# Performance work log

Hardware: AMD Instinct MI355X
Metric: run time of the kernel (lower is better)

Reference implementation:

```python
import jax, jax.numpy as jnp
import numpy as np

NEG_SLOPE_ATT = 0.2   # GATv2Conv attention leaky_relu slope
NEG_SLOPE_ACT = 0.01  # F.leaky_relu default between layers


def gatv2_layer(x, src, dst, edge_attr, Wl, Wr, We, att, concat):
    """PyG GATv2Conv (bias=False, residual=False, share_weights=False,
    add_self_loops=True with fill_value='mean' for edge_attr, eval mode)."""
    N = x.shape[0]
    H, C = att.shape
    E = src.shape[0]
    # self-loop edge attrs: mean of incoming edge attrs per node (fill_value='mean')
    deg = jax.ops.segment_sum(jnp.ones((E,), x.dtype), dst, num_segments=N)
    loop_attr = jax.ops.segment_sum(edge_attr, dst, num_segments=N) / jnp.maximum(deg, 1.0)[:, None]
    loop = jnp.arange(N)
    s = jnp.concatenate([src, loop])
    d = jnp.concatenate([dst, loop])
    ea = jnp.concatenate([edge_attr, loop_attr], axis=0)
    xl = (x @ Wl).reshape(N, H, C)  # lin_l -> source features (messages)
    xr = (x @ Wr).reshape(N, H, C)  # lin_r -> target features
    # edge-wise attention input: x_l[j] + x_r[i] + lin_edge(e_ij)  -> [E+N, H, C]
    e = xl[s] + xr[d] + (ea @ We).reshape(-1, H, C)
    e = jax.nn.leaky_relu(e, NEG_SLOPE_ATT)
    logits = jnp.einsum('ehc,hc->eh', e, att)  # [E+N, H]
    # numerically stable segment softmax over incoming edges per destination
    lmax = jax.ops.segment_max(logits, d, num_segments=N)  # every node has a self loop -> finite
    ex = jnp.exp(logits - lmax[d])
    denom = jax.ops.segment_sum(ex, d, num_segments=N)
    alpha = ex / (denom[d] + 1e-16)
    out = jax.ops.segment_sum(alpha[:, :, None] * xl[s], d, num_segments=N)  # [N, H, C]
    return out.reshape(N, H * C) if concat else out.mean(axis=1)


def setup_inputs() -> dict:
    key = jax.random.key(0)
    ks = jax.random.split(key, 12)
    N, E, F, H, C, EDIM, NCLS = 50000, 800000, 128, 4, 32, 16, 1
    HC = H * C  # 128
    sc = 0.1
    return {
        'x': jax.random.normal(ks[0], (N, F), jnp.float32),
        'edge_index': jax.random.randint(ks[1], (2, E), 0, N),
        'edge_attr': jax.random.normal(ks[2], (E, EDIM), jnp.float32),
        'Wl1': jax.random.normal(ks[3], (F, HC), jnp.float32) * sc,
        'Wr1': jax.random.normal(ks[4], (F, HC), jnp.float32) * sc,
        'We1': jax.random.normal(ks[5], (EDIM, HC), jnp.float32) * sc,
        'att1': jax.random.normal(ks[6], (H, C), jnp.float32) * sc,
        'Wl2': jax.random.normal(ks[7], (HC, H * NCLS), jnp.float32) * sc,
        'Wr2': jax.random.normal(ks[8], (HC, H * NCLS), jnp.float32) * sc,
        'We2': jax.random.normal(ks[9], (EDIM, H * NCLS), jnp.float32) * sc,
        'att2': jax.random.normal(ks[10], (H, NCLS), jnp.float32) * sc,
    }


def reference(x, edge_index, edge_attr, Wl1, Wr1, We1, att1, Wl2, Wr2, We2, att2):
    src, dst = edge_index[0], edge_index[1]
    h = gatv2_layer(x, src, dst, edge_attr, Wl1, Wr1, We1, att1, concat=True)
    h = jax.nn.leaky_relu(h, NEG_SLOPE_ACT)
    out = gatv2_layer(h, src, dst, edge_attr, Wl2, Wr2, We2, att2, concat=False)
    return out.reshape(-1)
```

## Files before the change

kernel.cpp:

```cpp
#include <hip/hip_runtime.h>
#include <math.h>


typedef __attribute__((ext_vector_type(8))) short bf16x8;
typedef __attribute__((ext_vector_type(4))) float f32x4;
typedef __attribute__((ext_vector_type(2))) float f32x2;
typedef _Float16 f16;
typedef __attribute__((ext_vector_type(2))) _Float16 f16x2;
typedef __attribute__((ext_vector_type(8))) _Float16 f16x8;

static __device__ __forceinline__ ushort f2bf(float f) {
    unsigned u = __float_as_uint(f);
    unsigned r = (u + 0x7fffu + ((u >> 16) & 1u)) >> 16;
    return (ushort)r;
}

static __device__ __forceinline__ float row_sum16(float x) {
    x += __int_as_float(__builtin_amdgcn_update_dpp(0, __float_as_int(x), 0x121, 0xf, 0xf, true));
    x += __int_as_float(__builtin_amdgcn_update_dpp(0, __float_as_int(x), 0x122, 0xf, 0xf, true));
    x += __int_as_float(__builtin_amdgcn_update_dpp(0, __float_as_int(x), 0x124, 0xf, 0xf, true));
    x += __int_as_float(__builtin_amdgcn_update_dpp(0, __float_as_int(x), 0x128, 0xf, 0xf, true));
    return x;
}

static __device__ __forceinline__ float red64(float x) {
    x = row_sum16(x);
    x += __shfl_xor(x, 16);
    x += __shfl_xor(x, 32);
    return x;
}

__global__ void k_count_deg(const int* __restrict__ dst, int* __restrict__ deg, int E) {
    int i = blockIdx.x * blockDim.x + threadIdx.x;
    if (i < E) atomicAdd(&deg[dst[i]], 1);
}

__global__ __launch_bounds__(1024) void k_scan1(const int* __restrict__ deg,
                                                int* __restrict__ rowptr,
                                                int* __restrict__ part, int N) {
    __shared__ int wsum[16];
    int t = threadIdx.x, l = t & 63, w = t >> 6;
    int i = blockIdx.x * 1024 + t;
    int v = (i < N) ? deg[i] : 0;
    int sc = v;
    #pragma unroll
    for (int off = 1; off < 64; off <<= 1) {
        int y = __shfl_up(sc, off);
        if (l >= off) sc += y;
    }
    if (l == 63) wsum[w] = sc;
    __syncthreads();
    if (w == 0) {
        int pv = (l < 16) ? wsum[l] : 0;
        int psc = pv;
        #pragma unroll
        for (int off = 1; off < 16; off <<= 1) {
            int y = __shfl_up(psc, off);
            if (l >= off) psc += y;
        }
        if (l < 16) wsum[l] = psc - pv;
    }
    __syncthreads();
    if (i < N) rowptr[i] = wsum[w] + sc - v;
    if (t == 1023) part[blockIdx.x] = wsum[15] + sc;
}

__global__ void k_scan2(int* __restrict__ part, int nb) {
    int l = threadIdx.x & 63;
    int run = 0;
    for (int base = 0; base < nb; base += 64) {
        int i = base + l;
        int v = (i < nb) ? part[i] : 0;
        int sc = v;
        #pragma unroll
        for (int off = 1; off < 64; off <<= 1) {
            int y = __shfl_up(sc, off);
            if (l >= off) sc += y;
        }
        if (i < nb) part[i] = run + sc - v;
        run += __shfl(sc, 63);
    }
}

__global__ void k_scan3(int* __restrict__ rowptr, const int* __restrict__ part, int N, int E) {
    int i = blockIdx.x * 256 + threadIdx.x;
    if (i < N) rowptr[i] += part[i >> 10];
    if (i == 0) rowptr[N] = E;
}

__global__ void k_scatter(const int* __restrict__ dst, const int* __restrict__ rowptr,
                          int* __restrict__ cursor, int* __restrict__ csr, int E) {
    int i = blockIdx.x * blockDim.x + threadIdx.x;
    if (i < E) {
        int d = dst[i];
        int pos = rowptr[d] + atomicAdd(&cursor[d], 1);
        csr[pos] = i;
    }
}

__global__ void k_wcvt(const float* __restrict__ Wl, const float* __restrict__ Wr,
                       const float* __restrict__ We1,
                       ushort* __restrict__ wcat, f16* __restrict__ we1h) {
    int i = blockIdx.x * 256 + threadIdx.x;
    if (i < 16 * 128) we1h[i] = (f16)We1[i];
    if (i >= 128 * 256) return;
    int k = i >> 8, n = i & 255;
    float v = (n < 128) ? Wl[k * 128 + n] : Wr[k * 128 + (n - 128)];
    wcat[i] = f2bf(v);
}

__global__ __launch_bounds__(256) void k_gemm1_mfma(
    const float* __restrict__ x, const ushort* __restrict__ wcat,
    ushort* __restrict__ xl, float* __restrict__ xr, int N) {
    __shared__ ushort xs[64 * 128];
    int t = threadIdx.x, l = t & 63, w = t >> 6;
    int r0 = blockIdx.x * 64;
    bf16x8 bf[4][4];
    {
        int coln = w * 64 + (l & 15);
        int kr = (l >> 4) * 8;
        #pragma unroll
        for (int nt = 0; nt < 4; ++nt) {
            #pragma unroll
            for (int ks = 0; ks < 4; ++ks) {
                #pragma unroll
                for (int j = 0; j < 8; ++j)
                    bf[nt][ks][j] = (short)wcat[(ks * 32 + kr + j) * 256 + nt * 16 + coln];
            }
        }
    }
    #pragma unroll
    for (int it = 0; it < 4; ++it) {
        int slot = t + 256 * it;
        int row = slot >> 4, ch = slot & 15;
        int grow = r0 + row;
        float v0 = 0.f, v1 = 0.f, v2 = 0.f, v3 = 0.f, v4 = 0.f, v5 = 0.f, v6 = 0.f, v7 = 0.f;
        if (grow < N) {
            float4 a = *(const float4*)(x + (size_t)grow * 128 + ch * 8);
            float4 b = *(const float4*)(x + (size_t)grow * 128 + ch * 8 + 4);
            v0 = a.x; v1 = a.y; v2 = a.z; v3 = a.w;
            v4 = b.x; v5 = b.y; v6 = b.z; v7 = b.w;
        }
        bf16x8 tv;
        tv[0] = (short)f2bf(v0); tv[1] = (short)f2bf(v1);
        tv[2] = (short)f2bf(v2); tv[3] = (short)f2bf(v3);
        tv[4] = (short)f2bf(v4); tv[5] = (short)f2bf(v5);
        tv[6] = (short)f2bf(v6); tv[7] = (short)f2bf(v7);
        int ch2 = ch ^ (row & 15);
        *(bf16x8*)&xs[row * 128 + ch2 * 8] = tv;
    }
    __syncthreads();
    f32x4 acc[4][4];
    #pragma unroll
    for (int mt = 0; mt < 4; ++mt)
        #pragma unroll
        for (int nt = 0; nt < 4; ++nt)
            acc[mt][nt] = (f32x4){0.f, 0.f, 0.f, 0.f};
    #pragma unroll
    for (int ks = 0; ks < 4; ++ks) {
        bf16x8 af[4];
        #pragma unroll
        for (int mt = 0; mt < 4; ++mt) {
            int row = mt * 16 + (l & 15);
            int ch = (ks * 4 + (l >> 4)) ^ (row & 15);
            af[mt] = *(const bf16x8*)&xs[row * 128 + ch * 8];
        }
        #pragma unroll
        for (int mt = 0; mt < 4; ++mt)
            #pragma unroll
            for (int nt = 0; nt < 4; ++nt)
                acc[mt][nt] = __builtin_amdgcn_mfma_f32_16x16x32_bf16(
                    af[mt], bf[nt][ks], acc[mt][nt], 0, 0, 0);
    }
    #pragma unroll
    for (int mt = 0; mt < 4; ++mt) {
        #pragma unroll
        for (int nt = 0; nt < 4; ++nt) {
            int colg = w * 64 + nt * 16 + (l & 15);
            #pragma unroll
            for (int r = 0; r < 4; ++r) {
                int rowg = r0 + mt * 16 + (l >> 4) * 4 + r;
                if (rowg < N) {
                    float val = acc[mt][nt][r];
                    if (colg < 128) xl[(size_t)rowg * 128 + colg] = f2bf(val);
                    else            xr[(size_t)rowg * 128 + (colg - 128)] = val;
                }
            }
        }
    }
}

__global__ __launch_bounds__(256) void k_eperm(
    const int* __restrict__ csr, const int* __restrict__ src,
    const float* __restrict__ ea, const float* __restrict__ We2,
    f16* __restrict__ ea_f16, float* __restrict__ qe2,
    int* __restrict__ src_perm, int E) {
    __shared__ float sW[64];
    int t = threadIdx.x;
    if (t < 64) sW[t] = We2[t];
    __syncthreads();
    int j = blockIdx.x * 256 + t;
    if (j >= E) return;
    int e = csr[j];
    src_perm[j] = src[e];
    const float4* s4 = (const float4*)(ea + (size_t)e * 16);
    float4 r0 = s4[0], r1 = s4[1], r2 = s4[2], r3 = s4[3];
    f16x8 h0, h1;
    h0[0] = (f16)r0.x; h0[1] = (f16)r0.y; h0[2] = (f16)r0.z; h0[3] = (f16)r0.w;
    h0[4] = (f16)r1.x; h0[5] = (f16)r1.y; h0[6] = (f16)r1.z; h0[7] = (f16)r1.w;
    h1[0] = (f16)r2.x; h1[1] = (f16)r2.y; h1[2] = (f16)r2.z; h1[3] = (f16)r2.w;
    h1[4] = (f16)r3.x; h1[5] = (f16)r3.y; h1[6] = (f16)r3.z; h1[7] = (f16)r3.w;
    *(f16x8*)(ea_f16 + (size_t)j * 16) = h0;
    *(f16x8*)(ea_f16 + (size_t)j * 16 + 8) = h1;
    float a[16] = {r0.x, r0.y, r0.z, r0.w, r1.x, r1.y, r1.z, r1.w,
                   r2.x, r2.y, r2.z, r2.w, r3.x, r3.y, r3.z, r3.w};
    float q0 = 0.f, q1 = 0.f, q2v = 0.f, q3 = 0.f;
    #pragma unroll
    for (int k = 0; k < 16; ++k) {
        q0 += a[k] * sW[k * 4 + 0];
        q1 += a[k] * sW[k * 4 + 1];
        q2v += a[k] * sW[k * 4 + 2];
        q3 += a[k] * sW[k * 4 + 3];
    }
    *(float4*)(qe2 + (size_t)j * 4) = make_float4(q0, q1, q2v, q3);
}

__global__ __launch_bounds__(256, 4) void k_fused1_dot(
    const int* __restrict__ rowptr, const int* __restrict__ src_perm,
    const ushort* __restrict__ xl_bf, const float* __restrict__ xr,
    const f16* __restrict__ ea_f16, const f16* __restrict__ we1h,
    const float* __restrict__ att,
    const float* __restrict__ Wl2, const float* __restrict__ Wr2,
    float* __restrict__ xl2, float* __restrict__ xr2, int N) {
    int t = threadIdx.x, l = t & 63;
    int n = (blockIdx.x * 256 + t) >> 6;
    if (n >= N) return;
    const float RLN2 = 1.44269504f;
    const unsigned* xlw = (const unsigned*)xl_bf;
    f16x2 weX[8], weY[8];
    #pragma unroll
    for (int kp = 0; kp < 8; ++kp) {
        weX[kp][0] = we1h[(2 * kp) * 128 + 2 * l];
        weX[kp][1] = we1h[(2 * kp + 1) * 128 + 2 * l];
        weY[kp][0] = we1h[(2 * kp) * 128 + 2 * l + 1];
        weY[kp][1] = we1h[(2 * kp + 1) * 128 + 2 * l + 1];
    }
    f32x2 av = *(const f32x2*)(att + 2 * l);
    av = av * RLN2;
    f32x2 xrv = *(const f32x2*)(xr + (size_t)n * 128 + 2 * l);
    int rs = rowptr[n], re = rowptr[n + 1];
    int deg = re - rs;
    int urs = __builtin_amdgcn_readfirstlane(rs);
    f32x2 acc = {0.f, 0.f}, mq = {0.f, 0.f};
    float den = 0.f;
    #pragma unroll 2
    for (int slot = 0; slot < deg; ++slot) {
        int jj = urs + slot;
        const f16x2* ap = (const f16x2*)(ea_f16 + (size_t)(unsigned)jj * 16);
        int s = src_perm[jj];
        unsigned xw = xlw[(unsigned)s * 64u + (unsigned)l];
        float qx = 0.f, qy = 0.f;
        #pragma unroll
        for (int kp = 0; kp < 8; ++kp) {
            f16x2 a = ap[kp];
            qx = __builtin_amdgcn_fdot2(a, weX[kp], qx, false);
            qy = __builtin_amdgcn_fdot2(a, weY[kp], qy, false);
        }
        f32x2 q = {qx, qy};
        f32x2 xlv;
        xlv.x = __uint_as_float(xw << 16);
        xlv.y = __uint_as_float(xw & 0xffff0000u);
        f32x2 v = xrv + q + xlv;
        f32x2 u = __builtin_elementwise_max(v, 0.2f * v);
        f32x2 pt = av * u;
        float p = row_sum16(pt.x + pt.y);
        float w = exp2f(p);
        acc += xlv * w;
        den += w;
        mq += q;
    }
    {
        float inv = 1.f / (float)(deg > 1 ? deg : 1);
        f32x2 q = mq * inv;
        unsigned xw = xlw[(unsigned)n * 64u + (unsigned)l];
        f32x2 xlv;
        xlv.x = __uint_as_float(xw << 16);
        xlv.y = __uint_as_float(xw & 0xffff0000u);
        f32x2 v = xrv + q + xlv;
        f32x2 u = __builtin_elementwise_max(v, 0.2f * v);
        f32x2 pt = av * u;
        float p = row_sum16(pt.x + pt.y);
        float w = exp2f(p);
        acc += xlv * w;
        den += w;
    }
    float rdn = 1.f / (den + 1e-16f);
    float h0 = acc.x * rdn, h1 = acc.y * rdn;
    h0 = h0 > 0.f ? h0 : 0.01f * h0;
    h1 = h1 > 0.f ? h1 : 0.01f * h1;
    float4 wla = *(const float4*)(Wl2 + (size_t)(2 * l) * 4);
    float4 wlb = *(const float4*)(Wl2 + (size_t)(2 * l + 1) * 4);
    float4 wra = *(const float4*)(Wr2 + (size_t)(2 * l) * 4);
    float4 wrb = *(const float4*)(Wr2 + (size_t)(2 * l + 1) * 4);
    float q0 = red64(h0 * wla.x + h1 * wlb.x);
    float q1 = red64(h0 * wla.y + h1 * wlb.y);
    float q2 = red64(h0 * wla.z + h1 * wlb.z);
    float q3 = red64(h0 * wla.w + h1 * wlb.w);
    float q4 = red64(h0 * wra.x + h1 * wrb.x);
    float q5 = red64(h0 * wra.y + h1 * wrb.y);
    float q6 = red64(h0 * wra.z + h1 * wrb.z);
    float q7 = red64(h0 * wra.w + h1 * wrb.w);
    if (l == 0) {
        *(float4*)(xl2 + (size_t)n * 4) = make_float4(q0, q1, q2, q3);
        *(float4*)(xr2 + (size_t)n * 4) = make_float4(q4, q5, q6, q7);
    }
}

__global__ __launch_bounds__(256, 4) void k_fused2_q(
    const int* __restrict__ rowptr, const int* __restrict__ src_perm,
    const float* __restrict__ xl2, const float* __restrict__ xr2,
    const float* __restrict__ qe2, const float* __restrict__ att2,
    float* __restrict__ out, int N) {
    int t = threadIdx.x, l = t & 63, g = l & 15;
    int node = (((blockIdx.x * 256 + t) >> 6) << 2) + (l >> 4);
    if (node >= N) return;
    int rs = rowptr[node], re = rowptr[node + 1];
    int deg = re - rs;
    float4 xrv = *(const float4*)(xr2 + (size_t)node * 4);
    const float RLN2 = 1.44269504f;
    float a0 = att2[0] * RLN2, a1 = att2[1] * RLN2;
    float a2 = att2[2] * RLN2, a3 = att2[3] * RLN2;
    float ac0 = 0.f, ac1 = 0.f, ac2 = 0.f, ac3 = 0.f;
    float dn0 = 0.f, dn1 = 0.f, dn2 = 0.f, dn3 = 0.f;
    float mq0 = 0.f, mq1 = 0.f, mq2 = 0.f, mq3 = 0.f;
    for (int slot = g; slot < deg; slot += 16) {
        int row = rs + slot;
        int s = src_perm[row];
        float4 q = *(const float4*)(qe2 + (size_t)row * 4);
        float4 xv = *(const float4*)(xl2 + (size_t)s * 4);
        float v0 = xv.x + xrv.x + q.x; v0 = fmaxf(v0, 0.2f * v0);
        float v1 = xv.y + xrv.y + q.y; v1 = fmaxf(v1, 0.2f * v1);
        float v2 = xv.z + xrv.z + q.z; v2 = fmaxf(v2, 0.2f * v2);
        float v3 = xv.w + xrv.w + q.w; v3 = fmaxf(v3, 0.2f * v3);
        float w0 = exp2f(v0 * a0); ac0 += w0 * xv.x; dn0 += w0;
        float w1 = exp2f(v1 * a1); ac1 += w1 * xv.y; dn1 += w1;
        float w2 = exp2f(v2 * a2); ac2 += w2 * xv.z; dn2 += w2;
        float w3 = exp2f(v3 * a3); ac3 += w3 * xv.w; dn3 += w3;
        mq0 += q.x; mq1 += q.y; mq2 += q.z; mq3 += q.w;
    }
    ac0 = row_sum16(ac0); ac1 = row_sum16(ac1);
    ac2 = row_sum16(ac2); ac3 = row_sum16(ac3);
    dn0 = row_sum16(dn0); dn1 = row_sum16(dn1);
    dn2 = row_sum16(dn2); dn3 = row_sum16(dn3);
    mq0 = row_sum16(mq0); mq1 = row_sum16(mq1);
    mq2 = row_sum16(mq2); mq3 = row_sum16(mq3);
    {
        float inv = 1.f / (float)(deg > 1 ? deg : 1);
        float4 xv = *(const float4*)(xl2 + (size_t)node * 4);
        float v0 = xv.x + xrv.x + mq0 * inv; v0 = fmaxf(v0, 0.2f * v0);
        float v1 = xv.y + xrv.y + mq1 * inv; v1 = fmaxf(v1, 0.2f * v1);
        float v2 = xv.z + xrv.z + mq2 * inv; v2 = fmaxf(v2, 0.2f * v2);
        float v3 = xv.w + xrv.w + mq3 * inv; v3 = fmaxf(v3, 0.2f * v3);
        float w0 = exp2f(v0 * a0); ac0 += w0 * xv.x; dn0 += w0;
        float w1 = exp2f(v1 * a1); ac1 += w1 * xv.y; dn1 += w1;
        float w2 = exp2f(v2 * a2); ac2 += w2 * xv.z; dn2 += w2;
        float w3 = exp2f(v3 * a3); ac3 += w3 * xv.w; dn3 += w3;
    }
    if (g == 0) {
        float r = ac0 / (dn0 + 1e-16f) + ac1 / (dn1 + 1e-16f)
                + ac2 / (dn2 + 1e-16f) + ac3 / (dn3 + 1e-16f);
        out[node] = r * 0.25f;
    }
}

extern "C" void kernel_launch(void* const* d_in, const int* in_sizes, int n_in,
                              void* d_out, int out_size, void* d_ws, size_t ws_size,
                              hipStream_t stream) {
    const float* x         = (const float*)d_in[0];
    const int*   edge_index= (const int*)d_in[1];
    const float* edge_attr = (const float*)d_in[2];
    const float* Wl1       = (const float*)d_in[3];
    const float* Wr1       = (const float*)d_in[4];
    const float* We1       = (const float*)d_in[5];
    const float* att1      = (const float*)d_in[6];
    const float* Wl2       = (const float*)d_in[7];
    const float* Wr2       = (const float*)d_in[8];
    const float* We2       = (const float*)d_in[9];
    const float* att2      = (const float*)d_in[10];
    float* outp = (float*)d_out;

    const int F = 128, HC = 128;
    int N = in_sizes[0] / F;
    int E = in_sizes[1] / 2;
    const int* src = edge_index;
    const int* dst = edge_index + E;

    char* ws = (char*)d_ws;
    size_t off = 0;
    auto alloc = [&](size_t bytes) {
        char* p = ws + off;
        off += (bytes + 255) & ~(size_t)255;
        return p;
    };
    int*      deg      = (int*)alloc((size_t)N * 4);
    int*      cursor   = (int*)alloc((size_t)N * 4);
    int*      rowptr   = (int*)alloc((size_t)(N + 1) * 4);
    int*      part     = (int*)alloc(((size_t)N / 1024 + 2) * 4);
    int*      csr      = (int*)alloc((size_t)E * 4);
    ushort*   wcat     = (ushort*)alloc((size_t)128 * 256 * 2);
    f16*      we1h     = (f16*)alloc((size_t)16 * 128 * 2);
    ushort*   xl_bf    = (ushort*)alloc((size_t)N * HC * 2);
    float*    xr1      = (float*)alloc((size_t)N * HC * 4);
    float*    xl2      = (float*)alloc((size_t)N * 4 * 4);
    float*    xr2      = (float*)alloc((size_t)N * 4 * 4);
    int*      src_perm = (int*)alloc((size_t)E * 4);
    float*    qe2      = (float*)alloc((size_t)E * 4 * 4);
    f16*      ea_f16   = (f16*)alloc((size_t)E * 16 * 2);

    int eb = (E + 255) / 256;
    int nb = (N + 1023) / 1024;

    hipMemsetAsync(deg, 0, (size_t)((char*)rowptr - (char*)deg), stream);
    k_count_deg<<<eb, 256, 0, stream>>>(dst, deg, E);
    k_scan1<<<nb, 1024, 0, stream>>>(deg, rowptr, part, N);
    k_scan2<<<1, 64, 0, stream>>>(part, nb);
    k_scan3<<<(N + 255) / 256, 256, 0, stream>>>(rowptr, part, N, E);
    k_scatter<<<eb, 256, 0, stream>>>(dst, rowptr, cursor, csr, E);
    k_wcvt<<<128, 256, 0, stream>>>(Wl1, Wr1, We1, wcat, we1h);
    k_gemm1_mfma<<<(N + 63) / 64, 256, 0, stream>>>(x, wcat, xl_bf, xr1, N);
    k_eperm<<<eb, 256, 0, stream>>>(csr, src, edge_attr, We2, ea_f16, qe2, src_perm, E);
    k_fused1_dot<<<(N + 3) / 4, 256, 0, stream>>>(rowptr, src_perm, xl_bf, xr1, ea_f16,
                                                  we1h, att1, Wl2, Wr2, xl2, xr2, N);
    k_fused2_q<<<(N + 15) / 16, 256, 0, stream>>>(rowptr, src_perm, xl2, xr2, qe2,
                                                  att2, outp, N);
}
```

Measured before the change: 247.5 us.

## Fuse CSR scatter with edge permutation and batch edge loads in layer-1 aggregation

The CSR scatter kernel and the edge-permutation kernel are merged, so each edge writes its source index, fp16 edge attributes and layer-2 edge projection straight to its CSR slot. This removes the intermediate csr index array, one kernel launch, and the gathered reads of edge_attr by permuted index. In exchange, the writes become scattered and the reads become coalesced. The layer-1 fused aggregation loop now processes edges in groups of four, issuing vectorized 16-byte edge-attribute loads and the source-row gathers up front to get more memory-level parallelism, at the cost of higher register pressure.

```diff
diff --git a/kernel.cpp b/kernel.cpp
--- a/kernel.cpp
+++ b/kernel.cpp
@@ -88,14 +88,41 @@
     if (i == 0) rowptr[N] = E;
 }
 
-__global__ void k_scatter(const int* __restrict__ dst, const int* __restrict__ rowptr,
-                          int* __restrict__ cursor, int* __restrict__ csr, int E) {
-    int i = blockIdx.x * blockDim.x + threadIdx.x;
-    if (i < E) {
-        int d = dst[i];
-        int pos = rowptr[d] + atomicAdd(&cursor[d], 1);
-        csr[pos] = i;
-    }
+__global__ __launch_bounds__(256) void k_scatter_e(
+    const int* __restrict__ dst, const int* __restrict__ src,
+    const float* __restrict__ ea, const float* __restrict__ We2,
+    const int* __restrict__ rowptr, int* __restrict__ cursor,
+    f16* __restrict__ ea_f16, float* __restrict__ qe2,
+    int* __restrict__ src_perm, int E) {
+    __shared__ float sW[64];
+    int t = threadIdx.x;
+    if (t < 64) sW[t] = We2[t];
+    __syncthreads();
+    int i = blockIdx.x * 256 + t;
+    if (i >= E) return;
+    int d = dst[i];
+    int pos = rowptr[d] + atomicAdd(&cursor[d], 1);
+    src_perm[pos] = src[i];
+    const float4* s4 = (const float4*)(ea + (size_t)i * 16);
+    float4 r0 = s4[0], r1 = s4[1], r2 = s4[2], r3 = s4[3];
+    f16x8 h0, h1;
+    h0[0] = (f16)r0.x; h0[1] = (f16)r0.y; h0[2] = (f16)r0.z; h0[3] = (f16)r0.w;
+    h0[4] = (f16)r1.x; h0[5] = (f16)r1.y; h0[6] = (f16)r1.z; h0[7] = (f16)r1.w;
+    h1[0] = (f16)r2.x; h1[1] = (f16)r2.y; h1[2] = (f16)r2.z; h1[3] = (f16)r2.w;
+    h1[4] = (f16)r3.x; h1[5] = (f16)r3.y; h1[6] = (f16)r3.z; h1[7] = (f16)r3.w;
+    *(f16x8*)(ea_f16 + (size_t)pos * 16) = h0;
+    *(f16x8*)(ea_f16 + (size_t)pos * 16 + 8) = h1;
+    float a[16] = {r0.x, r0.y, r0.z, r0.w, r1.x, r1.y, r1.z, r1.w,
+                   r2.x, r2.y, r2.z, r2.w, r3.x, r3.y, r3.z, r3.w};
+    float q0 = 0.f, q1 = 0.f, q2v = 0.f, q3 = 0.f;
+    #pragma unroll
+    for (int k = 0; k < 16; ++k) {
+        q0 += a[k] * sW[k * 4 + 0];
+        q1 += a[k] * sW[k * 4 + 1];
+        q2v += a[k] * sW[k * 4 + 2];
+        q3 += a[k] * sW[k * 4 + 3];
+    }
+    *(float4*)(qe2 + (size_t)pos * 4) = make_float4(q0, q1, q2v, q3);
 }
 
 __global__ void k_wcvt(const float* __restrict__ Wl, const float* __restrict__ Wr,
@@ -188,41 +215,6 @@
             }
         }
     }
-}
-
-__global__ __launch_bounds__(256) void k_eperm(
-    const int* __restrict__ csr, const int* __restrict__ src,
-    const float* __restrict__ ea, const float* __restrict__ We2,
-    f16* __restrict__ ea_f16, float* __restrict__ qe2,
-    int* __restrict__ src_perm, int E) {
-    __shared__ float sW[64];
-    int t = threadIdx.x;
-    if (t < 64) sW[t] = We2[t];
-    __syncthreads();
-    int j = blockIdx.x * 256 + t;
-    if (j >= E) return;
-    int e = csr[j];
-    src_perm[j] = src[e];
-    const float4* s4 = (const float4*)(ea + (size_t)e * 16);
-    float4 r0 = s4[0], r1 = s4[1], r2 = s4[2], r3 = s4[3];
-    f16x8 h0, h1;
-    h0[0] = (f16)r0.x; h0[1] = (f16)r0.y; h0[2] = (f16)r0.z; h0[3] = (f16)r0.w;
-    h0[4] = (f16)r1.x; h0[5] = (f16)r1.y; h0[6] = (f16)r1.z; h0[7] = (f16)r1.w;
-    h1[0] = (f16)r2.x; h1[1] = (f16)r2.y; h1[2] = (f16)r2.z; h1[3] = (f16)r2.w;
-    h1[4] = (f16)r3.x; h1[5] = (f16)r3.y; h1[6] = (f16)r3.z; h1[7] = (f16)r3.w;
-    *(f16x8*)(ea_f16 + (size_t)j * 16) = h0;
-    *(f16x8*)(ea_f16 + (size_t)j * 16 + 8) = h1;
-    float a[16] = {r0.x, r0.y, r0.z, r0.w, r1.x, r1.y, r1.z, r1.w,
-                   r2.x, r2.y, r2.z, r2.w, r3.x, r3.y, r3.z, r3.w};
-    float q0 = 0.f, q1 = 0.f, q2v = 0.f, q3 = 0.f;
-    #pragma unroll
-    for (int k = 0; k < 16; ++k) {
-        q0 += a[k] * sW[k * 4 + 0];
-        q1 += a[k] * sW[k * 4 + 1];
-        q2v += a[k] * sW[k * 4 + 2];
-        q3 += a[k] * sW[k * 4 + 3];
-    }
-    *(float4*)(qe2 + (size_t)j * 4) = make_float4(q0, q1, q2v, q3);
 }
 
 __global__ __launch_bounds__(256, 4) void k_fused1_dot(
@@ -253,18 +245,67 @@
     int urs = __builtin_amdgcn_readfirstlane(rs);
     f32x2 acc = {0.f, 0.f}, mq = {0.f, 0.f};
     float den = 0.f;
-    #pragma unroll 2
-    for (int slot = 0; slot < deg; ++slot) {
-        int jj = urs + slot;
-        const f16x2* ap = (const f16x2*)(ea_f16 + (size_t)(unsigned)jj * 16);
+    int full = deg & ~3;
+    for (int base = 0; base < full; base += 4) {
+        unsigned jj = (unsigned)(urs + base);
+        f16x8 ea0[4], ea1[4];
+        int sA[4];
+        #pragma unroll
+        for (int c = 0; c < 4; ++c) {
+            ea0[c] = *(const f16x8*)(ea_f16 + (size_t)(jj + c) * 16);
+            ea1[c] = *(const f16x8*)(ea_f16 + (size_t)(jj + c) * 16 + 8);
+            sA[c] = src_perm[jj + c];
+        }
+        unsigned xw[4];
+        #pragma unroll
+        for (int c = 0; c < 4; ++c) xw[c] = xlw[(unsigned)sA[c] * 64u + (unsigned)l];
+        #pragma unroll
+        for (int c = 0; c < 4; ++c) {
+            const f16x2* ap0 = (const f16x2*)&ea0[c];
+            const f16x2* ap1 = (const f16x2*)&ea1[c];
+            float qx = 0.f, qy = 0.f;
+            #pragma unroll
+            for (int kp = 0; kp < 4; ++kp) {
+                qx = __builtin_amdgcn_fdot2(ap0[kp], weX[kp], qx, false);
+                qy = __builtin_amdgcn_fdot2(ap0[kp], weY[kp], qy, false);
+            }
+            #pragma unroll
+            for (int kp = 0; kp < 4; ++kp) {
+                qx = __builtin_amdgcn_fdot2(ap1[kp], weX[4 + kp], qx, false);
+                qy = __builtin_amdgcn_fdot2(ap1[kp], weY[4 + kp], qy, false);
+            }
+            f32x2 q = {qx, qy};
+            f32x2 xlv;
+            xlv.x = __uint_as_float(xw[c] << 16);
+            xlv.y = __uint_as_float(xw[c] & 0xffff0000u);
+            f32x2 v = xrv + q + xlv;
+            f32x2 u = __builtin_elementwise_max(v, 0.2f * v);
+            f32x2 pt = av * u;
+            float p = row_sum16(pt.x + pt.y);
+            float w = exp2f(p);
+            acc += xlv * w;
+            den += w;
+            mq += q;
+        }
+    }
+    for (int slot = full; slot < deg; ++slot) {
+        unsigned jj = (unsigned)(urs + slot);
+        f16x8 e0 = *(const f16x8*)(ea_f16 + (size_t)jj * 16);
+        f16x8 e1 = *(const f16x8*)(ea_f16 + (size_t)jj * 16 + 8);
         int s = src_perm[jj];
         unsigned xw = xlw[(unsigned)s * 64u + (unsigned)l];
+        const f16x2* ap0 = (const f16x2*)&e0;
+        const f16x2* ap1 = (const f16x2*)&e1;
         float qx = 0.f, qy = 0.f;
         #pragma unroll
-        for (int kp = 0; kp < 8; ++kp) {
-            f16x2 a = ap[kp];
-            qx = __builtin_amdgcn_fdot2(a, weX[kp], qx, false);
-            qy = __builtin_amdgcn_fdot2(a, weY[kp], qy, false);
+        for (int kp = 0; kp < 4; ++kp) {
+            qx = __builtin_amdgcn_fdot2(ap0[kp], weX[kp], qx, false);
+            qy = __builtin_amdgcn_fdot2(ap0[kp], weY[kp], qy, false);
+        }
+        #pragma unroll
+        for (int kp = 0; kp < 4; ++kp) {
+            qx = __builtin_amdgcn_fdot2(ap1[kp], weX[4 + kp], qx, false);
+            qy = __builtin_amdgcn_fdot2(ap1[kp], weY[4 + kp], qy, false);
         }
         f32x2 q = {qx, qy};
         f32x2 xlv;
@@ -406,7 +447,6 @@
     int*      cursor   = (int*)alloc((size_t)N * 4);
     int*      rowptr   = (int*)alloc((size_t)(N + 1) * 4);
     int*      part     = (int*)alloc(((size_t)N / 1024 + 2) * 4);
-    int*      csr      = (int*)alloc((size_t)E * 4);
     ushort*   wcat     = (ushort*)alloc((size_t)128 * 256 * 2);
     f16*      we1h     = (f16*)alloc((size_t)16 * 128 * 2);
     ushort*   xl_bf    = (ushort*)alloc((size_t)N * HC * 2);
@@ -425,10 +465,10 @@
     k_scan1<<<nb, 1024, 0, stream>>>(deg, rowptr, part, N);
     k_scan2<<<1, 64, 0, stream>>>(part, nb);
     k_scan3<<<(N + 255) / 256, 256, 0, stream>>>(rowptr, part, N, E);
-    k_scatter<<<eb, 256, 0, stream>>>(dst, rowptr, cursor, csr, E);
+    k_scatter_e<<<eb, 256, 0, stream>>>(dst, src, edge_attr, We2, rowptr, cursor,
+                                        ea_f16, qe2, src_perm, E);
     k_wcvt<<<128, 256, 0, stream>>>(Wl1, Wr1, We1, wcat, we1h);
     k_gemm1_mfma<<<(N + 63) / 64, 256, 0, stream>>>(x, wcat, xl_bf, xr1, N);
-    k_eperm<<<eb, 256, 0, stream>>>(csr, src, edge_attr, We2, ea_f16, qe2, src_perm, E);
     k_fused1_dot<<<(N + 3) / 4, 256, 0, stream>>>(rowptr, src_perm, xl_bf, xr1, ea_f16,
                                                   we1h, att1, Wl2, Wr2, xl2, xr2, N);
     k_fused2_q<<<(N + 15) / 16, 256, 0, stream>>>(rowptr, src_perm, xl2, xr2, qe2,
```

After: 222.9 us. 1.11x faster.
